# Optimization experiments

Hardware: AMD Instinct MI355X
Metric: run time of the kernel (lower is better)

Reference implementation:

```python
import jax, jax.numpy as jnp
import numpy as np

K_RATIO = 0.7  # initial_ratio at epoch 0

def setup_inputs() -> dict:
    key = jax.random.key(0)
    k1, k2, k3 = jax.random.split(key, 3)
    B, D, C = 65536, 512, 1000
    features = jax.random.normal(k1, (B, D), dtype=jnp.float32)
    targets = jax.random.randint(k2, (B,), 0, C, dtype=jnp.int64)
    W = jax.random.normal(k3, (D, C), dtype=jnp.float32) / np.sqrt(D)
    b = jnp.zeros((C,), dtype=jnp.float32)
    return {"features": features, "targets": targets, "W": W, "b": b}

def reference(features, targets, W, b):
    # model: linear classifier -> logits [B, C]
    logits = features @ W + b
    # per-sample cross-entropy (reduction='none')
    logp = jax.nn.log_softmax(logits, axis=-1)
    losses = -jnp.take_along_axis(logp, targets[:, None], axis=-1)[:, 0]  # [B]
    B = features.shape[0]
    num_ohem = int(B * K_RATIO)
    # top-k hard examples, mean of their losses
    top_vals, _ = jax.lax.top_k(losses, num_ohem)
    return top_vals.mean()
```

## Files before the change

kernel.cpp:

```cpp
#include <hip/hip_runtime.h>
#include <hip/hip_bf16.h>

#define BTOT 65536
#define DDIM 512
#define CDIM 1000
#define KSEL 45875

#define L2E 1.44269504088896340736f
#define LN2 0.69314718055994530942f
#define NEG_BIG -1.0e30f

typedef __attribute__((ext_vector_type(8))) short short8;
typedef __attribute__((ext_vector_type(8))) unsigned short ushort8;
typedef __attribute__((ext_vector_type(4))) float f32x4;

__device__ __forceinline__ unsigned short f2bf(float f) {
  unsigned u = __float_as_uint(f);
  u += 0x7FFFu + ((u >> 16) & 1u);
  return (unsigned short)(u >> 16);
}

__device__ __forceinline__ short8 cvt8(const float4 f0, const float4 f1) {
  short8 v;
  v[0] = (short)f2bf(f0.x); v[1] = (short)f2bf(f0.y);
  v[2] = (short)f2bf(f0.z); v[3] = (short)f2bf(f0.w);
  v[4] = (short)f2bf(f1.x); v[5] = (short)f2bf(f1.y);
  v[6] = (short)f2bf(f1.z); v[7] = (short)f2bf(f1.w);
  return v;
}

__device__ __forceinline__ void gload_lds16(const void* g, void* l) {
  __builtin_amdgcn_global_load_lds(
      (const __attribute__((address_space(1))) unsigned int*)g,
      (__attribute__((address_space(3))) unsigned int*)l, 16, 0, 0);
}

__global__ void prep_all(const float* __restrict__ W, const float* __restrict__ b,
                         unsigned short* __restrict__ Wg, float* __restrict__ bp,
                         unsigned* __restrict__ hzero) {
  const int bid = blockIdx.x, tid = threadIdx.x;
  if (bid < 256) {
    const int idx = bid * 256 + tid;
    const int c  = idx & 1023;
    const int k8 = idx >> 10;
    const int p = c >> 4, cc = c & 15;
    ushort8 v;
#pragma unroll
    for (int j = 0; j < 8; ++j) {
      const int k = k8 * 8 + j;
      v[j] = (c < CDIM) ? f2bf(W[k * CDIM + c]) : (unsigned short)0;
    }
    const unsigned off = ((((unsigned)cc) << 10) | (((unsigned)k8) << 4)) ^
                         ((((unsigned)cc) & 7u) << 4);
    *(ushort8*)((char*)Wg + (size_t)p * 16384 + off) = v;
  } else if (bid < 384) {
    ((uint4*)hzero)[(bid - 256) * 256 + tid] = (uint4){0, 0, 0, 0};
  } else {
    for (int i = tid; i < 1024; i += 256) bp[i] = (i < CDIM) ? b[i] * L2E : NEG_BIG;
  }
}

__launch_bounds__(128)
__global__ void ohem_losses(const float* __restrict__ feat,
                            const int* __restrict__ targets,
                            const unsigned short* __restrict__ Wg,
                            const float* __restrict__ bpad,
                            float* __restrict__ losses,
                            unsigned* __restrict__ histHi) {
  __shared__ char lbuf[2][16384];
  __shared__ float biasLds[1024];
  const int tid = threadIdx.x, lane = tid & 63, w = tid >> 6;
  const int l15 = lane & 15, lgrp = lane >> 4;
  const int rowB = blockIdx.x * 64 + w * 32;

#pragma unroll
  for (int j = 0; j < 8; ++j) biasLds[tid * 8 + j] = bpad[tid * 8 + j];

#pragma unroll
  for (int r = 0; r < 8; ++r) {
    const int off = (r * 128 + tid) * 16;
    gload_lds16((const char*)Wg + off, &lbuf[0][0] + off);
  }

  short8 a[2][16];
#pragma unroll
  for (int rf = 0; rf < 2; ++rf) {
    const float* src = feat + (size_t)(rowB + rf * 16 + l15) * DDIM + lgrp * 8;
#pragma unroll
    for (int ks = 0; ks < 16; ++ks) {
      const float4 f0 = *(const float4*)(src + ks * 32);
      const float4 f1 = *(const float4*)(src + ks * 32 + 4);
      a[rf][ks] = cvt8(f0, f1);
    }
  }

  int   tcol[8];
  float s[8], tv[8];
#pragma unroll
  for (int rf = 0; rf < 2; ++rf)
#pragma unroll
    for (int r = 0; r < 4; ++r) {
      const int slot = rf * 4 + r;
      tcol[slot] = targets[rowB + rf * 16 + lgrp * 4 + r];
      s[slot] = 0.f; tv[slot] = NEG_BIG;
    }

  __syncthreads();

  const unsigned xm   = ((unsigned)(l15 & 7)) << 4;
  const unsigned bofs = (((unsigned)l15) << 10) | (((unsigned)lgrp) << 4);

  for (int nc = 0; nc < 64; ++nc) {
    const int cur = nc & 1;
    if (nc + 1 < 64) {
      const char* src = (const char*)Wg + (size_t)(nc + 1) * 16384;
#pragma unroll
      for (int r = 0; r < 8; ++r) {
        const int off = (r * 128 + tid) * 16;
        gload_lds16(src + off, &lbuf[cur ^ 1][0] + off);
      }
    }

    f32x4 acc0 = (f32x4){0.f, 0.f, 0.f, 0.f};
    f32x4 acc1 = (f32x4){0.f, 0.f, 0.f, 0.f};
    const char* lb = &lbuf[cur][0];
#pragma unroll
    for (int ks = 0; ks < 16; ++ks) {
      const short8 b0 = *(const short8*)(lb + ((bofs | ((unsigned)ks << 6)) ^ xm));
      acc0 = __builtin_amdgcn_mfma_f32_16x16x32_bf16(a[0][ks], b0, acc0, 0, 0, 0);
      acc1 = __builtin_amdgcn_mfma_f32_16x16x32_bf16(a[1][ks], b0, acc1, 0, 0, 0);
    }

    const int col0 = (nc << 4) + l15;
    const float bb0 = biasLds[col0];
#pragma unroll
    for (int r = 0; r < 4; ++r) {
      const float z0 = fmaf(acc0[r], L2E, bb0);
      const float z1 = fmaf(acc1[r], L2E, bb0);
      if (col0 == tcol[r])     tv[r]     = z0;
      if (col0 == tcol[4 + r]) tv[4 + r] = z1;
      s[r]     += __builtin_amdgcn_exp2f(z0);
      s[4 + r] += __builtin_amdgcn_exp2f(z1);
    }

    __syncthreads();
  }

#pragma unroll
  for (int st = 1; st <= 8; st <<= 1)
#pragma unroll
    for (int slot = 0; slot < 8; ++slot) {
      s[slot] += __shfl_xor(s[slot], st, 64);
      tv[slot] = fmaxf(tv[slot], __shfl_xor(tv[slot], st, 64));
    }

  if (l15 == 0) {
#pragma unroll
    for (int rf = 0; rf < 2; ++rf)
#pragma unroll
      for (int r = 0; r < 4; ++r) {
        const int slot = rf * 4 + r;
        float loss = LN2 * (__builtin_amdgcn_logf(s[slot]) - tv[slot]);
        loss = fmaxf(loss, 0.f);
        losses[rowB + rf * 16 + lgrp * 4 + r] = loss;
        atomicAdd(&histHi[__float_as_uint(loss) >> 16], 1u);
      }
  }
}


__global__ void scan_level(const unsigned* __restrict__ hist,
                           unsigned* __restrict__ state, const int level) {
  const int t = threadIdx.x;
  __shared__ unsigned sh[256];
  const unsigned k       = (level == 0) ? (unsigned)KSEL : state[1];
  const unsigned oldpref = (level == 0) ? 0u : state[0];

  unsigned gs = 0;
  const uint4* hp = (const uint4*)(hist + t * 256);
#pragma unroll 4
  for (int i = 0; i < 64; ++i) { const uint4 h = hp[i]; gs += h.x + h.y + h.z + h.w; }
  sh[t] = gs;
  __syncthreads();
  for (int off = 1; off < 256; off <<= 1) {
    unsigned v = sh[t];
    if (t + off < 256) v += sh[t + off];
    __syncthreads();
    sh[t] = v;
    __syncthreads();
  }
  const unsigned incl  = sh[t];
  const unsigned above = (t < 255) ? sh[t + 1] : 0u;
  if (above < k && k <= incl) {
    unsigned kk = k - above;
    int bkt = 255;
    for (; bkt > 0; --bkt) {
      const unsigned c = hist[t * 256 + bkt];
      if (kk <= c) break;
      kk -= c;
    }
    const unsigned bin = (unsigned)(t * 256 + bkt);
    if (level == 0) { state[0] = bin << 16;      state[1] = kk; }
    else            { state[0] = oldpref | bin;  state[1] = kk; }
  }
}

__global__ void hist_lo(const float* __restrict__ losses,
                        const unsigned* __restrict__ state,
                        unsigned* __restrict__ hLo) {
  const unsigned pref = state[0] >> 16;
  const int i = blockIdx.x * 256 + threadIdx.x;
  const unsigned u = ((const unsigned*)losses)[i];
  if ((u >> 16) == pref) atomicAdd(&hLo[u & 0xFFFFu], 1u);
}

__global__ void ohem_sum(const float* __restrict__ losses,
                         const unsigned* __restrict__ state,
                         float* __restrict__ psum, unsigned* __restrict__ pcnt) {
  const unsigned ut = state[0];
  const int i = blockIdx.x * 256 + threadIdx.x;
  const float v = losses[i];
  const unsigned u = __float_as_uint(v);
  float    sv = (u > ut) ? v  : 0.f;
  unsigned sc = (u > ut) ? 1u : 0u;
#pragma unroll
  for (int st = 32; st >= 1; st >>= 1) {
    sv += __shfl_xor(sv, st, 64);
    sc += __shfl_xor(sc, st, 64);
  }
  __shared__ float    wsum[4];
  __shared__ unsigned wcnt[4];
  const int w = threadIdx.x >> 6;
  if ((threadIdx.x & 63) == 0) { wsum[w] = sv; wcnt[w] = sc; }
  __syncthreads();
  if (threadIdx.x == 0) {
    psum[blockIdx.x] = wsum[0] + wsum[1] + wsum[2] + wsum[3];
    pcnt[blockIdx.x] = wcnt[0] + wcnt[1] + wcnt[2] + wcnt[3];
  }
}

__global__ void ohem_final(const float* __restrict__ psum,
                           const unsigned* __restrict__ pcnt,
                           const unsigned* __restrict__ state,
                           float* __restrict__ out) {
  float    sv = psum[threadIdx.x];
  unsigned sc = pcnt[threadIdx.x];
#pragma unroll
  for (int st = 32; st >= 1; st >>= 1) {
    sv += __shfl_xor(sv, st, 64);
    sc += __shfl_xor(sc, st, 64);
  }
  __shared__ float    wsum[4];
  __shared__ unsigned wcnt[4];
  const int w = threadIdx.x >> 6;
  if ((threadIdx.x & 63) == 0) { wsum[w] = sv; wcnt[w] = sc; }
  __syncthreads();
  if (threadIdx.x == 0) {
    const float    sum = wsum[0] + wsum[1] + wsum[2] + wsum[3];
    const unsigned cnt = wcnt[0] + wcnt[1] + wcnt[2] + wcnt[3];
    const float t = __uint_as_float(state[0]);
    out[0] = (sum + (float)(KSEL - cnt) * t) / (float)KSEL;
  }
}

extern "C" void kernel_launch(void* const* d_in, const int* in_sizes, int n_in,
                              void* d_out, int out_size, void* d_ws, size_t ws_size,
                              hipStream_t stream) {
  const float* feat    = (const float*)d_in[0];
  const int*   targets = (const int*)d_in[1];
  const float* W       = (const float*)d_in[2];
  const float* b       = (const float*)d_in[3];
  float* out = (float*)d_out;

  char* ws = (char*)d_ws;
  unsigned short* Wg     = (unsigned short*)ws;
  float*          bp     = (float*)(ws + 1048576);
  float*          losses = (float*)(ws + 1052672);
  unsigned*       hHi    = (unsigned*)(ws + 1314816);
  unsigned*       hLo    = (unsigned*)(ws + 1576960);
  unsigned*       state  = (unsigned*)(ws + 1839104);
  float*          psum   = (float*)(ws + 1839360);
  unsigned*       pcnt   = (unsigned*)(ws + 1840384);

  prep_all<<<385, 256, 0, stream>>>(W, b, Wg, bp, hHi);
  ohem_losses<<<1024, 128, 0, stream>>>(feat, targets, Wg, bp, losses, hHi);
  scan_level<<<1, 256, 0, stream>>>(hHi, state, 0);
  hist_lo<<<256, 256, 0, stream>>>(losses, state, hLo);
  scan_level<<<1, 256, 0, stream>>>(hLo, state, 1);
  ohem_sum<<<256, 256, 0, stream>>>(losses, state, psum, pcnt);
  ohem_final<<<1, 256, 0, stream>>>(psum, pcnt, state, out);
}
```

Before: 343.0 us.

## Retile loss GEMM to 512-thread blocks with 32-column W chunks per stage

The classifier GEMM is retiled. Each block now has 8 waves covering 128 rows instead of 2 waves covering 64, each wave owns 16 rows instead of 32, and each pipeline stage streams 32 columns of W into LDS instead of 16. This halves the number of blocks, so W is staged from global memory half as many times in total, and it halves the number of barrier-separated stages. The cost is a larger LDS footprint per block, more waves sharing each barrier, and less A-fragment reuse per wave, since one A fragment now feeds two B fragments where before one B fed two A.

```diff
diff --git a/kernel.cpp b/kernel.cpp
--- a/kernel.cpp
+++ b/kernel.cpp
@@ -43,7 +43,7 @@
     const int idx = bid * 256 + tid;
     const int c  = idx & 1023;
     const int k8 = idx >> 10;
-    const int p = c >> 4, cc = c & 15;
+    const int p = c >> 5, cc = c & 31;
     ushort8 v;
 #pragma unroll
     for (int j = 0; j < 8; ++j) {
@@ -52,7 +52,7 @@
     }
     const unsigned off = ((((unsigned)cc) << 10) | (((unsigned)k8) << 4)) ^
                          ((((unsigned)cc) & 7u) << 4);
-    *(ushort8*)((char*)Wg + (size_t)p * 16384 + off) = v;
+    *(ushort8*)((char*)Wg + (size_t)p * 32768 + off) = v;
   } else if (bid < 384) {
     ((uint4*)hzero)[(bid - 256) * 256 + tid] = (uint4){0, 0, 0, 0};
   } else {
@@ -60,63 +60,59 @@
   }
 }
 
-__launch_bounds__(128)
+__launch_bounds__(512, 2)
 __global__ void ohem_losses(const float* __restrict__ feat,
                             const int* __restrict__ targets,
                             const unsigned short* __restrict__ Wg,
                             const float* __restrict__ bpad,
                             float* __restrict__ losses,
                             unsigned* __restrict__ histHi) {
-  __shared__ char lbuf[2][16384];
+  __shared__ char lbuf[2][32768];
   __shared__ float biasLds[1024];
   const int tid = threadIdx.x, lane = tid & 63, w = tid >> 6;
   const int l15 = lane & 15, lgrp = lane >> 4;
-  const int rowB = blockIdx.x * 64 + w * 32;
-
-#pragma unroll
-  for (int j = 0; j < 8; ++j) biasLds[tid * 8 + j] = bpad[tid * 8 + j];
-
-#pragma unroll
-  for (int r = 0; r < 8; ++r) {
-    const int off = (r * 128 + tid) * 16;
+  const int rowW = blockIdx.x * 128 + w * 16;
+
+  biasLds[tid * 2]     = bpad[tid * 2];
+  biasLds[tid * 2 + 1] = bpad[tid * 2 + 1];
+
+#pragma unroll
+  for (int r = 0; r < 4; ++r) {
+    const int off = (r * 512 + tid) * 16;
     gload_lds16((const char*)Wg + off, &lbuf[0][0] + off);
   }
 
-  short8 a[2][16];
-#pragma unroll
-  for (int rf = 0; rf < 2; ++rf) {
-    const float* src = feat + (size_t)(rowB + rf * 16 + l15) * DDIM + lgrp * 8;
+  short8 a[16];
+  {
+    const float* src = feat + (size_t)(rowW + l15) * DDIM + lgrp * 8;
 #pragma unroll
     for (int ks = 0; ks < 16; ++ks) {
       const float4 f0 = *(const float4*)(src + ks * 32);
       const float4 f1 = *(const float4*)(src + ks * 32 + 4);
-      a[rf][ks] = cvt8(f0, f1);
-    }
-  }
-
-  int   tcol[8];
-  float s[8], tv[8];
-#pragma unroll
-  for (int rf = 0; rf < 2; ++rf)
-#pragma unroll
-    for (int r = 0; r < 4; ++r) {
-      const int slot = rf * 4 + r;
-      tcol[slot] = targets[rowB + rf * 16 + lgrp * 4 + r];
-      s[slot] = 0.f; tv[slot] = NEG_BIG;
-    }
+      a[ks] = cvt8(f0, f1);
+    }
+  }
+
+  int   tcol[4];
+  float s[4], tv[4];
+#pragma unroll
+  for (int r = 0; r < 4; ++r) {
+    tcol[r] = targets[rowW + lgrp * 4 + r];
+    s[r] = 0.f; tv[r] = NEG_BIG;
+  }
 
   __syncthreads();
 
   const unsigned xm   = ((unsigned)(l15 & 7)) << 4;
   const unsigned bofs = (((unsigned)l15) << 10) | (((unsigned)lgrp) << 4);
 
-  for (int nc = 0; nc < 64; ++nc) {
+  for (int nc = 0; nc < 32; ++nc) {
     const int cur = nc & 1;
-    if (nc + 1 < 64) {
-      const char* src = (const char*)Wg + (size_t)(nc + 1) * 16384;
-#pragma unroll
-      for (int r = 0; r < 8; ++r) {
-        const int off = (r * 128 + tid) * 16;
+    if (nc + 1 < 32) {
+      const char* src = (const char*)Wg + (size_t)(nc + 1) * 32768;
+#pragma unroll
+      for (int r = 0; r < 4; ++r) {
+        const int off = (r * 512 + tid) * 16;
         gload_lds16(src + off, &lbuf[cur ^ 1][0] + off);
       }
     }
@@ -126,21 +122,24 @@
     const char* lb = &lbuf[cur][0];
 #pragma unroll
     for (int ks = 0; ks < 16; ++ks) {
-      const short8 b0 = *(const short8*)(lb + ((bofs | ((unsigned)ks << 6)) ^ xm));
-      acc0 = __builtin_amdgcn_mfma_f32_16x16x32_bf16(a[0][ks], b0, acc0, 0, 0, 0);
-      acc1 = __builtin_amdgcn_mfma_f32_16x16x32_bf16(a[1][ks], b0, acc1, 0, 0, 0);
-    }
-
-    const int col0 = (nc << 4) + l15;
+      const unsigned o0 = (bofs | ((unsigned)ks << 6)) ^ xm;
+      const short8 b0 = *(const short8*)(lb + o0);
+      const short8 b1 = *(const short8*)(lb + o0 + 16384u);
+      acc0 = __builtin_amdgcn_mfma_f32_16x16x32_bf16(a[ks], b0, acc0, 0, 0, 0);
+      acc1 = __builtin_amdgcn_mfma_f32_16x16x32_bf16(a[ks], b1, acc1, 0, 0, 0);
+    }
+
+    const int col0 = (nc << 5) + l15;
+    const int col1 = col0 + 16;
     const float bb0 = biasLds[col0];
+    const float bb1 = biasLds[col1];
 #pragma unroll
     for (int r = 0; r < 4; ++r) {
       const float z0 = fmaf(acc0[r], L2E, bb0);
-      const float z1 = fmaf(acc1[r], L2E, bb0);
-      if (col0 == tcol[r])     tv[r]     = z0;
-      if (col0 == tcol[4 + r]) tv[4 + r] = z1;
-      s[r]     += __builtin_amdgcn_exp2f(z0);
-      s[4 + r] += __builtin_amdgcn_exp2f(z1);
+      const float z1 = fmaf(acc1[r], L2E, bb1);
+      if (col0 == tcol[r]) tv[r] = z0;
+      if (col1 == tcol[r]) tv[r] = z1;
+      s[r] += __builtin_amdgcn_exp2f(z0) + __builtin_amdgcn_exp2f(z1);
     }
 
     __syncthreads();
@@ -149,25 +148,21 @@
 #pragma unroll
   for (int st = 1; st <= 8; st <<= 1)
 #pragma unroll
-    for (int slot = 0; slot < 8; ++slot) {
-      s[slot] += __shfl_xor(s[slot], st, 64);
-      tv[slot] = fmaxf(tv[slot], __shfl_xor(tv[slot], st, 64));
+    for (int r = 0; r < 4; ++r) {
+      s[r] += __shfl_xor(s[r], st, 64);
+      tv[r] = fmaxf(tv[r], __shfl_xor(tv[r], st, 64));
     }
 
   if (l15 == 0) {
 #pragma unroll
-    for (int rf = 0; rf < 2; ++rf)
-#pragma unroll
-      for (int r = 0; r < 4; ++r) {
-        const int slot = rf * 4 + r;
-        float loss = LN2 * (__builtin_amdgcn_logf(s[slot]) - tv[slot]);
-        loss = fmaxf(loss, 0.f);
-        losses[rowB + rf * 16 + lgrp * 4 + r] = loss;
-        atomicAdd(&histHi[__float_as_uint(loss) >> 16], 1u);
-      }
-  }
-}
-
+    for (int r = 0; r < 4; ++r) {
+      float loss = LN2 * (__builtin_amdgcn_logf(s[r]) - tv[r]);
+      loss = fmaxf(loss, 0.f);
+      losses[rowW + lgrp * 4 + r] = loss;
+      atomicAdd(&histHi[__float_as_uint(loss) >> 16], 1u);
+    }
+  }
+}
 
 __global__ void scan_level(const unsigned* __restrict__ hist,
                            unsigned* __restrict__ state, const int level) {
@@ -283,7 +278,7 @@
   unsigned*       pcnt   = (unsigned*)(ws + 1840384);
 
   prep_all<<<385, 256, 0, stream>>>(W, b, Wg, bp, hHi);
-  ohem_losses<<<1024, 128, 0, stream>>>(feat, targets, Wg, bp, losses, hHi);
+  ohem_losses<<<512, 512, 0, stream>>>(feat, targets, Wg, bp, losses, hHi);
   scan_level<<<1, 256, 0, stream>>>(hHi, state, 0);
   hist_lo<<<256, 256, 0, stream>>>(losses, state, hLo);
   scan_level<<<1, 256, 0, stream>>>(hLo, state, 1);
```

Result: faster. 310.5 us (-9.5%).
